# Optimization experiments

Hardware: AMD Instinct MI355X
Metric: run time of the kernel (lower is better)

Reference implementation:

```python
import jax, jax.numpy as jnp
import numpy as np

HIDDEN = 1024
N_HEADS = 16
HEAD_DIM = HIDDEN // N_HEADS


def setup_inputs() -> dict:
    key = jax.random.key(0)
    ks = jax.random.split(key, 8)
    bs, seq = 8, 1024
    hidden_states = jax.random.normal(ks[0], (bs, seq, HIDDEN), dtype=jnp.float32)
    attention_mask = jnp.zeros((bs, 1, 1, seq), dtype=jnp.float32)
    s = 1.0 / np.sqrt(HIDDEN)
    Wq = jax.random.normal(ks[1], (HIDDEN, HIDDEN), dtype=jnp.float32) * s
    bq = jnp.zeros((HIDDEN,), dtype=jnp.float32)
    Wk = jax.random.normal(ks[2], (HIDDEN, HIDDEN), dtype=jnp.float32) * s
    bk = jnp.zeros((HIDDEN,), dtype=jnp.float32)
    Wv = jax.random.normal(ks[3], (HIDDEN, HIDDEN), dtype=jnp.float32) * s
    bv = jnp.zeros((HIDDEN,), dtype=jnp.float32)
    return {"hidden_states": hidden_states, "attention_mask": attention_mask,
            "Wq": Wq, "bq": bq, "Wk": Wk, "bk": bk, "Wv": Wv, "bv": bv}


def _split_heads(x):
    # [b, s, H] -> [b, h, s, d]
    b, s, _ = x.shape
    return x.reshape(b, s, N_HEADS, HEAD_DIM).transpose(0, 2, 1, 3)


def reference(hidden_states, attention_mask, Wq, bq, Wk, bk, Wv, bv):
    q = _split_heads(hidden_states @ Wq.T + bq)
    k = _split_heads(hidden_states @ Wk.T + bk)
    v = _split_heads(hidden_states @ Wv.T + bv)
    scale = 1.0 / np.sqrt(HEAD_DIM).astype(np.float32)
    scores = jnp.einsum('bhqd,bhkd->bhqk', q, k) * scale + attention_mask
    probs = jax.nn.softmax(scores, axis=-1)  # dropout p=0.0 -> identity
    ctx = jnp.einsum('bhqk,bhkd->bhqd', probs, v)
    b, h, s, d = ctx.shape
    return ctx.transpose(0, 2, 1, 3).reshape(b, s, h * d)
```

## Files before the change

### kernel.cpp

```cpp
#include <hip/hip_runtime.h>
#include <stdint.h>
#include <stddef.h>

#define HIDDEN 1024
#define NHEADS 16
#define HDIM   64
#define BS     8
#define SEQ    1024
#define MTOT   (BS*SEQ)
#define QKV_T  ((size_t)MTOT*HIDDEN)

typedef short    bf16x8 __attribute__((ext_vector_type(8)));
typedef short    bf16x4 __attribute__((ext_vector_type(4)));
typedef float    f32x4  __attribute__((ext_vector_type(4)));
typedef uint16_t u16x4  __attribute__((ext_vector_type(4)));

__device__ __forceinline__ uint16_t f2bf(float f) {
  union { float f; uint32_t u; } c; c.f = f;
  uint32_t u = c.u + 0x7FFFu + ((c.u >> 16) & 1u);
  return (uint16_t)(u >> 16);
}

__device__ __forceinline__ uint32_t cvt_pk_bf16(float lo, float hi) {
  uint32_t r;
  asm("v_cvt_pk_bf16_f32 %0, %1, %2" : "=v"(r) : "v"(lo), "v"(hi));
  return r;
}

__device__ __forceinline__ bf16x4 pack_bf16x4(float a, float b, float c, float d) {
  union { uint2 u; bf16x4 v; } cv;
  cv.u.x = cvt_pk_bf16(a, b);
  cv.u.y = cvt_pk_bf16(c, d);
  return cv.v;
}

__device__ __forceinline__ f32x4 mfma_16x16x16(bf16x4 a, bf16x4 b, f32x4 c) {
#if __has_builtin(__builtin_amdgcn_mfma_f32_16x16x16bf16_1k)
  return __builtin_amdgcn_mfma_f32_16x16x16bf16_1k(a, b, c, 0, 0, 0);
#elif __has_builtin(__builtin_amdgcn_mfma_f32_16x16x16_bf16)
  return __builtin_amdgcn_mfma_f32_16x16x16_bf16(a, b, c, 0, 0, 0);
#else
  f32x4 d;
  asm("v_mfma_f32_16x16x16_bf16 %0, %1, %2, %3"
      : "=&v"(d) : "v"(a), "v"(b), "v"(c));
  return d;
#endif
}

__device__ __forceinline__ float exp2fast(float x) {
#if __has_builtin(__builtin_amdgcn_exp2f)
  return __builtin_amdgcn_exp2f(x);
#else
  return __expf(x * 0.69314718056f);
#endif
}

__device__ __forceinline__ void gload_lds16(const uint16_t* g, uint16_t* lds) {
  __builtin_amdgcn_global_load_lds(
      (const __attribute__((address_space(1))) uint32_t*)g,
      (__attribute__((address_space(3))) uint32_t*)lds, 16, 0, 0);
}

__global__ __launch_bounds__(256) void cvt_kernel(
    const float* __restrict__ hs, const float* __restrict__ wq,
    const float* __restrict__ wk, const float* __restrict__ wv,
    uint16_t* __restrict__ hsb, uint16_t* __restrict__ wcat)
{
  const int i4 = blockIdx.x * 256 + threadIdx.x;
  f32x4 v;
  u16x4 o;
  if (i4 < 2097152) {
    v = *((const f32x4*)hs + i4);
    o[0]=f2bf(v[0]); o[1]=f2bf(v[1]); o[2]=f2bf(v[2]); o[3]=f2bf(v[3]);
    *((u16x4*)hsb + i4) = o;
  } else {
    int j4 = i4 - 2097152;
    int w  = j4 >> 18;
    int r4 = j4 & 262143;
    const float* src = (w == 0) ? wq : ((w == 1) ? wk : wv);
    v = *((const f32x4*)src + r4);
    o[0]=f2bf(v[0]); o[1]=f2bf(v[1]); o[2]=f2bf(v[2]); o[3]=f2bf(v[3]);
    *((u16x4*)wcat + j4) = o;
  }
}

__global__ __launch_bounds__(256) void gemm_qkv(
    const uint16_t* __restrict__ hsb, const uint16_t* __restrict__ wcat,
    const float* __restrict__ bq, const float* __restrict__ bk,
    const float* __restrict__ bv, uint16_t* __restrict__ qbuf,
    uint16_t* __restrict__ kbuf, uint16_t* __restrict__ vtbuf)
{
  __shared__ uint16_t Alds[2][128*32];
  __shared__ uint16_t Blds[2][128*32];

  const int bid = blockIdx.x;
  const int wg  = (bid & 7) * 192 + (bid >> 3);
  const int tm  = wg / 24, tn = wg % 24;
  const int m0  = tm * 128, n0 = tn * 128;
  const int t   = threadIdx.x;
  const int l   = t & 63, w = t >> 6;
  const int wm  = w >> 1, wn = w & 1;

  f32x4 acc[4][4];
#pragma unroll
  for (int i = 0; i < 4; i++)
#pragma unroll
    for (int j = 0; j < 4; j++) acc[i][j] = (f32x4){0.f,0.f,0.f,0.f};

  const int r0   = (w * 2) * 16 + (l >> 2);
  const int r1   = (w * 2 + 1) * 16 + (l >> 2);
  const int g0s  = (l & 3) ^ ((r0 >> 1) & 3);
  const int g1s  = (l & 3) ^ ((r1 >> 1) & 3);
  const size_t aoff0 = (size_t)r0 * HIDDEN + g0s * 8;
  const size_t aoff1 = (size_t)r1 * HIDDEN + g1s * 8;

  auto STAGE = [&](int buf, int kt) {
    const uint16_t* Ab = hsb  + (size_t)m0 * HIDDEN + kt * 32;
    const uint16_t* Bb = wcat + (size_t)n0 * HIDDEN + kt * 32;
    gload_lds16(Ab + aoff0, &Alds[buf][(w * 2) * 512]);
    gload_lds16(Ab + aoff1, &Alds[buf][(w * 2 + 1) * 512]);
    gload_lds16(Bb + aoff0, &Blds[buf][(w * 2) * 512]);
    gload_lds16(Bb + aoff1, &Blds[buf][(w * 2 + 1) * 512]);
  };

  auto COMPUTE = [&](int buf) {
    bf16x8 af[4], bfr[4];
    const int G = l >> 4;
#pragma unroll
    for (int i = 0; i < 4; i++) {
      int ar = wm * 64 + i * 16 + (l & 15);
      int gs = (G ^ ((ar >> 1) & 3)) & 3;
      af[i] = *(const bf16x8*)&Alds[buf][ar * 32 + gs * 8];
    }
#pragma unroll
    for (int j = 0; j < 4; j++) {
      int br = wn * 64 + j * 16 + (l & 15);
      int gs = (G ^ ((br >> 1) & 3)) & 3;
      bfr[j] = *(const bf16x8*)&Blds[buf][br * 32 + gs * 8];
    }
#pragma unroll
    for (int i = 0; i < 4; i++)
#pragma unroll
      for (int j = 0; j < 4; j++)
        acc[i][j] = __builtin_amdgcn_mfma_f32_16x16x32_bf16(af[i], bfr[j], acc[i][j], 0, 0, 0);
  };

  STAGE(0, 0);
  STAGE(1, 1);
#pragma unroll 1
  for (int kt = 0; kt < 32; ++kt) {
    if (kt < 31) { asm volatile("s_waitcnt vmcnt(4)" ::: "memory"); }
    else         { asm volatile("s_waitcnt vmcnt(0)" ::: "memory"); }
    __builtin_amdgcn_s_barrier();
    __builtin_amdgcn_sched_barrier(0);
    COMPUTE(kt & 1);
    if (kt < 31) {
      __builtin_amdgcn_s_barrier();
      __builtin_amdgcn_sched_barrier(0);
      if (kt < 30) STAGE(kt & 1, kt + 2);
    }
  }

#pragma unroll
  for (int j = 0; j < 4; j++) {
    int n     = n0 + wn * 64 + j * 16 + (l & 15);
    int which = n >> 10, nn = n & 1023;
    const float* bp = (which == 0) ? bq : ((which == 1) ? bk : bv);
    float bias = bp[nn];
    int hh = nn >> 6, dd = nn & 63;
#pragma unroll
    for (int i = 0; i < 4; i++) {
      if (which == 2) {
        int m_  = m0 + wm * 64 + i * 16 + (l >> 4) * 4;
        int b_  = m_ >> 10, s_ = m_ & 1023;
        size_t bhh = (size_t)(b_ * NHEADS + hh);
        uint2 pk;
        pk.x = cvt_pk_bf16(acc[i][j][0] + bias, acc[i][j][1] + bias);
        pk.y = cvt_pk_bf16(acc[i][j][2] + bias, acc[i][j][3] + bias);
        *(uint2*)&vtbuf[(bhh * HDIM + dd) * SEQ + s_] = pk;
      } else {
#pragma unroll
        for (int r = 0; r < 4; r++) {
          int m  = m0 + wm * 64 + i * 16 + (l >> 4) * 4 + r;
          int b_ = m >> 10, s_ = m & 1023;
          float val = acc[i][j][r] + bias;
          size_t bhh = (size_t)(b_ * NHEADS + hh);
          if (which == 0)
            qbuf[(bhh * SEQ + s_) * HDIM + dd] = f2bf(val * 0.18033688011112042f);
          else
            kbuf[(bhh * SEQ + s_) * HDIM + dd] = f2bf(val);
        }
      }
    }
  }
}

__global__ __launch_bounds__(256) void attn_kernel(
    const uint16_t* __restrict__ qb, const uint16_t* __restrict__ kb,
    const uint16_t* __restrict__ vtb, const float* __restrict__ mask,
    float* __restrict__ out)
{
  __shared__ uint16_t Klds[64 * 64];
  __shared__ uint16_t Vlds[64 * 64];
  __shared__ float    mlds[SEQ];

  const int bid = blockIdx.x;
  const int wg  = (bid & 7) * 128 + (bid >> 3);
  const int bh  = wg >> 3;
  const int qt  = wg & 7;
  const int b   = bh >> 4, h = bh & 15;

  const uint16_t* Qg = qb  + (size_t)bh * SEQ * HDIM;
  const uint16_t* Kg = kb  + (size_t)bh * SEQ * HDIM;
  const uint16_t* Vg = vtb + (size_t)bh * HDIM * SEQ;

  const int t = threadIdx.x, l = t & 63, w = t >> 6;
  const int G = l >> 4, q16 = l & 15;

  for (int i = t; i < SEQ; i += 256)
    mlds[i] = mask[b * SEQ + i] * 1.44269504089f;

  const int q0w = qt * 128 + w * 32;
  bf16x8 qf[2][2];
#pragma unroll
  for (int qi = 0; qi < 2; ++qi)
#pragma unroll
    for (int k0 = 0; k0 < 2; ++k0)
      qf[qi][k0] = *(const bf16x8*)(Qg + (size_t)(q0w + qi * 16 + q16) * HDIM + k0 * 32 + G * 8);

  f32x4 O[4][2];
#pragma unroll
  for (int dt = 0; dt < 4; dt++) { O[dt][0] = (f32x4){0,0,0,0}; O[dt][1] = (f32x4){0,0,0,0}; }
  float mrow[2] = {-3e38f, -3e38f}, lrow[2] = {0.f, 0.f};

  const int srow8 = l >> 3;
  const int gsrc  = (l & 7) ^ srow8;
  const int qsw = q16 & 7;

  __syncthreads();

#pragma unroll 1
  for (int kt = 0; kt < 16; ++kt) {
#pragma unroll
    for (int ia = 0; ia < 2; ia++) {
      const int rbase = ia * 32 + w * 8;
      const int row   = rbase + srow8;
      gload_lds16(Kg + (size_t)(kt * 64 + row) * HDIM + gsrc * 8, &Klds[rbase * 64]);
      gload_lds16(Vg + (size_t)row * SEQ + kt * 64 + gsrc * 8,    &Vlds[rbase * 64]);
    }
    __syncthreads();

    f32x4 mv[4];
#pragma unroll
    for (int jn = 0; jn < 4; jn++)
      mv[jn] = *(const f32x4*)&mlds[kt * 64 + jn * 16 + G * 4];

    bf16x4 pa[2][4];

#pragma unroll
    for (int qi = 0; qi < 2; ++qi) {
      f32x4 sc[4];
#pragma unroll
      for (int jn = 0; jn < 4; jn++) sc[jn] = (f32x4){0,0,0,0};
#pragma unroll
      for (int k0 = 0; k0 < 2; ++k0)
#pragma unroll
        for (int jn = 0; jn < 4; jn++) {
          int kr = jn * 16 + q16;
          int gs = ((k0 * 4 + G) ^ qsw) & 7;
          bf16x8 kf = *(const bf16x8*)&Klds[kr * 64 + gs * 8];
          sc[jn] = __builtin_amdgcn_mfma_f32_16x16x32_bf16(kf, qf[qi][k0], sc[jn], 0, 0, 0);
        }

      float pm = -3e38f;
#pragma unroll
      for (int jn = 0; jn < 4; jn++) {
        sc[jn] += mv[jn];
        pm = fmaxf(pm, fmaxf(fmaxf(sc[jn][0], sc[jn][1]), fmaxf(sc[jn][2], sc[jn][3])));
      }
      pm = fmaxf(pm, __shfl_xor(pm, 16));
      pm = fmaxf(pm, __shfl_xor(pm, 32));
      if (!__all(pm <= mrow[qi] + 11.0f)) {
        float mn = fmaxf(mrow[qi], pm);
        float fs = exp2fast(mrow[qi] - mn);
        mrow[qi] = mn;
        lrow[qi] *= fs;
#pragma unroll
        for (int dt = 0; dt < 4; dt++) O[dt][qi] *= fs;
      }
      float ps = 0.f;
#pragma unroll
      for (int jn = 0; jn < 4; jn++) {
        float p0 = exp2fast(sc[jn][0] - mrow[qi]);
        float p1 = exp2fast(sc[jn][1] - mrow[qi]);
        float p2 = exp2fast(sc[jn][2] - mrow[qi]);
        float p3 = exp2fast(sc[jn][3] - mrow[qi]);
        ps += (p0 + p1) + (p2 + p3);
        pa[qi][jn] = pack_bf16x4(p0, p1, p2, p3);
      }
      ps += __shfl_xor(ps, 16);
      ps += __shfl_xor(ps, 32);
      lrow[qi] += ps;
    }

#pragma unroll
    for (int jn = 0; jn < 4; jn++) {
      const int gq = 2 * jn + (G >> 1);
#pragma unroll
      for (int dt = 0; dt < 4; dt++) {
        const int dr   = dt * 16 + q16;
        const int slot = gq ^ (dr & 7);
        bf16x4 vf = *(const bf16x4*)&Vlds[dr * 64 + slot * 8 + (G & 1) * 4];
        O[dt][0] = mfma_16x16x16(vf, pa[0][jn], O[dt][0]);
        O[dt][1] = mfma_16x16x16(vf, pa[1][jn], O[dt][1]);
      }
    }
    __syncthreads();
  }

#pragma unroll
  for (int qi = 0; qi < 2; ++qi) {
    float inv = 1.0f / lrow[qi];
    int q = q0w + qi * 16 + q16;
    float* orow = out + (size_t)(b * SEQ + q) * HIDDEN + h * HDIM;
#pragma unroll
    for (int dt = 0; dt < 4; dt++) {
      f32x4 o4 = O[dt][qi] * inv;
      *(f32x4*)(orow + dt * 16 + G * 4) = o4;
    }
  }
}

extern "C" void kernel_launch(void* const* d_in, const int* in_sizes, int n_in,
                              void* d_out, int out_size, void* d_ws, size_t ws_size,
                              hipStream_t stream) {
  const float* hs   = (const float*)d_in[0];
  const float* mask = (const float*)d_in[1];
  const float* Wq   = (const float*)d_in[2];
  const float* bq   = (const float*)d_in[3];
  const float* Wk   = (const float*)d_in[4];
  const float* bk   = (const float*)d_in[5];
  const float* Wv   = (const float*)d_in[6];
  const float* bv   = (const float*)d_in[7];
  float* out = (float*)d_out;

  uint16_t* hsb  = (uint16_t*)d_ws;
  uint16_t* wcat = (uint16_t*)((char*)d_ws + 16777216u);
  uint16_t* qbuf = (uint16_t*)((char*)d_ws + 23068672u);
  uint16_t* kbuf = (uint16_t*)((char*)d_ws + 39845888u);
  uint16_t* vtbf = (uint16_t*)((char*)d_ws + 56623104u);

  cvt_kernel<<<11264, 256, 0, stream>>>(hs, Wq, Wk, Wv, hsb, wcat);
  gemm_qkv<<<1536, 256, 0, stream>>>(hsb, wcat, bq, bk, bv, qbuf, kbuf, vtbf);
  attn_kernel<<<1024, 256, 0, stream>>>(qbuf, kbuf, vtbf, mask, out);
}
```

Baseline: 151.5 us.

## Double attention KV tile to 128 keys and interleave Q-row score MFMAs

The attention kernel now processes 128 keys per iteration instead of 64, halving the number of loop iterations and barriers. K and V LDS tiles double in size, and the V layout uses a 16-slot XOR swizzle for the wider rows. The QK^T MFMAs for both query groups are issued together so each K fragment is loaded once, and softmax is factored into a lambda. This raises register pressure (sixteen score vectors live at once) and LDS use, which may reduce occupancy.

```diff
diff --git a/kernel.cpp b/kernel.cpp
--- a/kernel.cpp
+++ b/kernel.cpp
@@ -200,8 +200,8 @@
     const uint16_t* __restrict__ vtb, const float* __restrict__ mask,
     float* __restrict__ out)
 {
-  __shared__ uint16_t Klds[64 * 64];
-  __shared__ uint16_t Vlds[64 * 64];
+  __shared__ uint16_t Klds[128 * 64];
+  __shared__ uint16_t Vlds[64 * 128];
   __shared__ float    mlds[SEQ];
 
   const int bid = blockIdx.x;
@@ -228,105 +228,111 @@
     for (int k0 = 0; k0 < 2; ++k0)
       qf[qi][k0] = *(const bf16x8*)(Qg + (size_t)(q0w + qi * 16 + q16) * HDIM + k0 * 32 + G * 8);
 
-  f32x4 O[4][2];
-#pragma unroll
-  for (int dt = 0; dt < 4; dt++) { O[dt][0] = (f32x4){0,0,0,0}; O[dt][1] = (f32x4){0,0,0,0}; }
-  float mrow[2] = {-3e38f, -3e38f}, lrow[2] = {0.f, 0.f};
+  f32x4 O0[4], O1[4];
+#pragma unroll
+  for (int dt = 0; dt < 4; dt++) { O0[dt] = (f32x4){0,0,0,0}; O1[dt] = (f32x4){0,0,0,0}; }
+  float mrow0 = -3e38f, mrow1 = -3e38f, lrow0 = 0.f, lrow1 = 0.f;
 
   const int srow8 = l >> 3;
-  const int gsrc  = (l & 7) ^ srow8;
+  const int gsrcK = (l & 7) ^ srow8;
   const int qsw = q16 & 7;
 
+  auto softmax_q = [&](f32x4 (&scq)[8], bf16x4 (&paq)[8], float& mq, float& lq,
+                       f32x4 (&Oq)[4], int ktbase) {
+    float pm = -3e38f;
+#pragma unroll
+    for (int jn = 0; jn < 8; jn++) {
+      f32x4 mvj = *(const f32x4*)&mlds[ktbase + jn * 16 + G * 4];
+      scq[jn] += mvj;
+      pm = fmaxf(pm, fmaxf(fmaxf(scq[jn][0], scq[jn][1]), fmaxf(scq[jn][2], scq[jn][3])));
+    }
+    pm = fmaxf(pm, __shfl_xor(pm, 16));
+    pm = fmaxf(pm, __shfl_xor(pm, 32));
+    if (!__all(pm <= mq + 11.0f)) {
+      float mn = fmaxf(mq, pm);
+      float fs = exp2fast(mq - mn);
+      mq = mn; lq *= fs;
+#pragma unroll
+      for (int dt = 0; dt < 4; dt++) Oq[dt] *= fs;
+    }
+    float ps = 0.f;
+#pragma unroll
+    for (int jn = 0; jn < 8; jn++) {
+      float p0 = exp2fast(scq[jn][0] - mq);
+      float p1 = exp2fast(scq[jn][1] - mq);
+      float p2 = exp2fast(scq[jn][2] - mq);
+      float p3 = exp2fast(scq[jn][3] - mq);
+      ps += (p0 + p1) + (p2 + p3);
+      paq[jn] = pack_bf16x4(p0, p1, p2, p3);
+    }
+    ps += __shfl_xor(ps, 16);
+    ps += __shfl_xor(ps, 32);
+    lq += ps;
+  };
+
   __syncthreads();
 
 #pragma unroll 1
-  for (int kt = 0; kt < 16; ++kt) {
-#pragma unroll
-    for (int ia = 0; ia < 2; ia++) {
-      const int rbase = ia * 32 + w * 8;
-      const int row   = rbase + srow8;
-      gload_lds16(Kg + (size_t)(kt * 64 + row) * HDIM + gsrc * 8, &Klds[rbase * 64]);
-      gload_lds16(Vg + (size_t)row * SEQ + kt * 64 + gsrc * 8,    &Vlds[rbase * 64]);
+  for (int kt = 0; kt < 8; ++kt) {
+    const int ktbase = kt * 128;
+#pragma unroll
+    for (int ja = 0; ja < 4; ja++) {
+      const int rbK = ja * 32 + w * 8;
+      gload_lds16(Kg + (size_t)(ktbase + rbK + srow8) * HDIM + gsrcK * 8,
+                  &Klds[rbK * 64]);
+      const int rbV = ja * 16 + w * 4;
+      const int dV  = rbV + (l >> 4);
+      const int gV  = (l & 15) ^ (dV & 7);
+      gload_lds16(Vg + (size_t)dV * SEQ + ktbase + gV * 8,
+                  &Vlds[rbV * 128]);
     }
     __syncthreads();
 
-    f32x4 mv[4];
-#pragma unroll
-    for (int jn = 0; jn < 4; jn++)
-      mv[jn] = *(const f32x4*)&mlds[kt * 64 + jn * 16 + G * 4];
-
-    bf16x4 pa[2][4];
-
-#pragma unroll
-    for (int qi = 0; qi < 2; ++qi) {
-      f32x4 sc[4];
-#pragma unroll
-      for (int jn = 0; jn < 4; jn++) sc[jn] = (f32x4){0,0,0,0};
-#pragma unroll
-      for (int k0 = 0; k0 < 2; ++k0)
-#pragma unroll
-        for (int jn = 0; jn < 4; jn++) {
-          int kr = jn * 16 + q16;
-          int gs = ((k0 * 4 + G) ^ qsw) & 7;
-          bf16x8 kf = *(const bf16x8*)&Klds[kr * 64 + gs * 8];
-          sc[jn] = __builtin_amdgcn_mfma_f32_16x16x32_bf16(kf, qf[qi][k0], sc[jn], 0, 0, 0);
-        }
-
-      float pm = -3e38f;
-#pragma unroll
-      for (int jn = 0; jn < 4; jn++) {
-        sc[jn] += mv[jn];
-        pm = fmaxf(pm, fmaxf(fmaxf(sc[jn][0], sc[jn][1]), fmaxf(sc[jn][2], sc[jn][3])));
-      }
-      pm = fmaxf(pm, __shfl_xor(pm, 16));
-      pm = fmaxf(pm, __shfl_xor(pm, 32));
-      if (!__all(pm <= mrow[qi] + 11.0f)) {
-        float mn = fmaxf(mrow[qi], pm);
-        float fs = exp2fast(mrow[qi] - mn);
-        mrow[qi] = mn;
-        lrow[qi] *= fs;
-#pragma unroll
-        for (int dt = 0; dt < 4; dt++) O[dt][qi] *= fs;
-      }
-      float ps = 0.f;
-#pragma unroll
-      for (int jn = 0; jn < 4; jn++) {
-        float p0 = exp2fast(sc[jn][0] - mrow[qi]);
-        float p1 = exp2fast(sc[jn][1] - mrow[qi]);
-        float p2 = exp2fast(sc[jn][2] - mrow[qi]);
-        float p3 = exp2fast(sc[jn][3] - mrow[qi]);
-        ps += (p0 + p1) + (p2 + p3);
-        pa[qi][jn] = pack_bf16x4(p0, p1, p2, p3);
-      }
-      ps += __shfl_xor(ps, 16);
-      ps += __shfl_xor(ps, 32);
-      lrow[qi] += ps;
-    }
-
-#pragma unroll
-    for (int jn = 0; jn < 4; jn++) {
+    f32x4 sc0[8], sc1[8];
+#pragma unroll
+    for (int jn = 0; jn < 8; jn++) {
+      const int kr  = jn * 16 + q16;
+      const int gs0 = (G ^ qsw) & 7;
+      const int gs1 = ((4 + G) ^ qsw) & 7;
+      bf16x8 kf0 = *(const bf16x8*)&Klds[kr * 64 + gs0 * 8];
+      bf16x8 kf1 = *(const bf16x8*)&Klds[kr * 64 + gs1 * 8];
+      f32x4 z = (f32x4){0, 0, 0, 0};
+      sc0[jn] = __builtin_amdgcn_mfma_f32_16x16x32_bf16(kf0, qf[0][0], z, 0, 0, 0);
+      sc0[jn] = __builtin_amdgcn_mfma_f32_16x16x32_bf16(kf1, qf[0][1], sc0[jn], 0, 0, 0);
+      sc1[jn] = __builtin_amdgcn_mfma_f32_16x16x32_bf16(kf0, qf[1][0], z, 0, 0, 0);
+      sc1[jn] = __builtin_amdgcn_mfma_f32_16x16x32_bf16(kf1, qf[1][1], sc1[jn], 0, 0, 0);
+    }
+
+    bf16x4 pa0[8], pa1[8];
+    softmax_q(sc0, pa0, mrow0, lrow0, O0, ktbase);
+    softmax_q(sc1, pa1, mrow1, lrow1, O1, ktbase);
+
+#pragma unroll
+    for (int jn = 0; jn < 8; jn++) {
       const int gq = 2 * jn + (G >> 1);
 #pragma unroll
       for (int dt = 0; dt < 4; dt++) {
         const int dr   = dt * 16 + q16;
         const int slot = gq ^ (dr & 7);
-        bf16x4 vf = *(const bf16x4*)&Vlds[dr * 64 + slot * 8 + (G & 1) * 4];
-        O[dt][0] = mfma_16x16x16(vf, pa[0][jn], O[dt][0]);
-        O[dt][1] = mfma_16x16x16(vf, pa[1][jn], O[dt][1]);
+        bf16x4 vf = *(const bf16x4*)&Vlds[dr * 128 + slot * 8 + (G & 1) * 4];
+        O0[dt] = mfma_16x16x16(vf, pa0[jn], O0[dt]);
+        O1[dt] = mfma_16x16x16(vf, pa1[jn], O1[dt]);
       }
     }
     __syncthreads();
   }
 
-#pragma unroll
-  for (int qi = 0; qi < 2; ++qi) {
-    float inv = 1.0f / lrow[qi];
-    int q = q0w + qi * 16 + q16;
-    float* orow = out + (size_t)(b * SEQ + q) * HIDDEN + h * HDIM;
+  {
+    float inv0 = 1.0f / lrow0, inv1 = 1.0f / lrow1;
+    int qa = q0w + q16, qb2 = q0w + 16 + q16;
+    float* orow0 = out + (size_t)(b * SEQ + qa)  * HIDDEN + h * HDIM;
+    float* orow1 = out + (size_t)(b * SEQ + qb2) * HIDDEN + h * HDIM;
 #pragma unroll
     for (int dt = 0; dt < 4; dt++) {
-      f32x4 o4 = O[dt][qi] * inv;
-      *(f32x4*)(orow + dt * 16 + G * 4) = o4;
+      f32x4 a = O0[dt] * inv0;
+      f32x4 c = O1[dt] * inv1;
+      *(f32x4*)(orow0 + dt * 16 + G * 4) = a;
+      *(f32x4*)(orow1 + dt * 16 + G * 4) = c;
     }
   }
 }
```

After: 144.6 us. -4.6%, faster.
